# Kernel optimization log

Measured on AMD Instinct MI355X. Metric: run time of the kernel, lower is better.

The kernel has to match this reference:

```python
import jax, jax.numpy as jnp
import numpy as np

T, B, IN, H, A = 512, 256, 292, 128, 12


def setup_inputs() -> dict:
    key = jax.random.key(0)
    ks = jax.random.split(key, 8)
    s = 1.0 / np.sqrt(H)
    return {
        "x": jax.random.normal(ks[0], (T, B, IN), dtype=jnp.float32),
        "done": jax.random.randint(ks[1], (T, B), 0, 2, dtype=jnp.int32),
        "h0": jax.random.normal(ks[2], (1, B, H), dtype=jnp.float32),
        "c0": jax.random.normal(ks[3], (1, B, H), dtype=jnp.float32),
        "W_ih": jax.random.normal(ks[4], (4 * H, IN), dtype=jnp.float32) * s,
        "W_hh": jax.random.normal(ks[5], (4 * H, H), dtype=jnp.float32) * s,
        "b_ih": jnp.zeros((4 * H,), dtype=jnp.float32),
        "b_hh": jnp.zeros((4 * H,), dtype=jnp.float32),
        "W_pi": jax.random.normal(ks[6], (A, H), dtype=jnp.float32) * 0.01,
        "b_pi": jnp.zeros((A,), dtype=jnp.float32),
        "W_v": jax.random.normal(ks[7], (1, H), dtype=jnp.float32),
        "b_v": jnp.zeros((1,), dtype=jnp.float32),
    }


def reference(x, done, h0, c0, W_ih, W_hh, b_ih, b_hh, W_pi, b_pi, W_v, b_v):
    # get_states: per-timestep LSTM with done-based reset of (h, c), as a scan.
    done_f = done.astype(x.dtype)  # [T, B]
    bias = b_ih + b_hh  # [4H]

    def step(carry, inp):
        h, c = carry  # [B, H] each
        x_t, d_t = inp  # [B, IN], [B]
        m = (1.0 - d_t)[:, None]  # reset mask
        h = h * m
        c = c * m
        # PyTorch LSTM gate order: input, forget, cell(g), output
        gates = x_t @ W_ih.T + h @ W_hh.T + bias  # [B, 4H]
        i, f, g, o = jnp.split(gates, 4, axis=-1)
        c = jax.nn.sigmoid(f) * c + jax.nn.sigmoid(i) * jnp.tanh(g)
        h = jax.nn.sigmoid(o) * jnp.tanh(c)
        return (h, c), h

    (hN, cN), hs = jax.lax.scan(step, (h0[0], c0[0]), (x, done_f))
    hidden = hs.reshape(T * B, H)  # flatten(cat(new_hidden), 0, 1)
    logits = hidden @ W_pi.T + b_pi  # policy_layers
    value = hidden @ W_v.T + b_v  # value_layers
    return jnp.concatenate([logits, value], axis=-1)  # [T*B, A+1]
```

## Files before the change

### kernel.cpp

```cpp
#include <hip/hip_runtime.h>
#include <stdint.h>
#include <stddef.h>

#define T_ 512
#define B_ 256
#define IN_ 292
#define H_ 128
#define G4_ 512
#define TB_ 131072
#define LCH 32
#define NCH 16
#define KP_ 320

typedef short bf16x8 __attribute__((ext_vector_type(8)));
typedef float f32x4 __attribute__((ext_vector_type(4)));

__device__ __forceinline__ unsigned short f2bf(float f) {
  unsigned u = __float_as_uint(f);
  u += 0x7FFFu + ((u >> 16) & 1u);
  return (unsigned short)(u >> 16);
}
__device__ __forceinline__ float bf2f(unsigned short s) {
  return __uint_as_float(((unsigned)s) << 16);
}
__device__ __forceinline__ unsigned bfpack2(float a, float b) {
  unsigned ua = __float_as_uint(a) + 0x8000u;
  unsigned ub = __float_as_uint(b) + 0x8000u;
  return __builtin_amdgcn_perm(ub, ua, 0x07060302u);
}
__device__ __forceinline__ float sigf(float x) {
  return __builtin_amdgcn_rcpf(1.0f + __expf(-x));
}
__device__ __forceinline__ float tanhf_(float x) {
  return 1.0f - 2.0f * __builtin_amdgcn_rcpf(__expf(2.0f * x) + 1.0f);
}
__device__ __forceinline__ void barrier_lds() {
  asm volatile("s_waitcnt lgkmcnt(0)\n\ts_barrier" ::: "memory");
}
__device__ __forceinline__ void load_pr(const unsigned short* p, ushort4* pr) {
  union { uint4 v; ushort4 s[2]; } a, b;
  a.v = *(const uint4*)p;
  b.v = *(const uint4*)(p + 8);
  pr[0] = a.s[0]; pr[1] = a.s[1]; pr[2] = b.s[0]; pr[3] = b.s[1];
}

__global__ __launch_bounds__(256) void k0w_cvt(
    const float* __restrict__ Wih, const float* __restrict__ bih,
    const float* __restrict__ bhh, unsigned short* __restrict__ Wf,
    float* __restrict__ bias2) {
  const int g = blockIdx.x * 256 + threadIdx.x;
  const int lane = g & 63;
  const int rest = g >> 6;
  const int it = rest % 10;
  const int g16 = rest / 10;
  const int jj = g16 * 16 + (lane & 15);
  const int src = (jj & 3) * 128 + (jj >> 2);
  const int c0 = it * 32 + (lane >> 4) * 8;
  if (g < 512) {
    const int sb = (g & 3) * 128 + (g >> 2);
    bias2[g] = bih[sb] + bhh[sb];
  }
  float4 a = {0.f, 0.f, 0.f, 0.f}, b = {0.f, 0.f, 0.f, 0.f};
  const float* p = Wih + (size_t)src * IN_ + c0;
  if (c0 + 8 <= IN_) { a = *(const float4*)p; b = *(const float4*)(p + 4); }
  else if (c0 < IN_) { a = *(const float4*)p; }
  uint4 o;
  o.x = bfpack2(a.x, a.y); o.y = bfpack2(a.z, a.w);
  o.z = bfpack2(b.x, b.y); o.w = bfpack2(b.z, b.w);
  *(uint4*)&Wf[(size_t)g * 8] = o;
}

__device__ __forceinline__ void k1_xissue(
    const float* __restrict__ x, int bid4, int xrow, int xcq, int g2,
    float4* xa, float4* xbv) {
  const int jx = g2 / 10, itx = g2 % 10;
  const float* p = x + (size_t)((bid4 + jx) * 128 + xrow) * IN_ + itx * 32 + xcq;
  const float4 z = {0.f, 0.f, 0.f, 0.f};
  if (itx < 9) {
    xa[g2 & 1] = *(const float4*)p;
    xbv[g2 & 1] = *(const float4*)(p + 4);
  } else {
    xa[g2 & 1] = (xcq == 0) ? *(const float4*)p : z;
    xbv[g2 & 1] = z;
  }
}

__global__ __launch_bounds__(512, 2) void k1_pregemm(
    const float* __restrict__ x, const unsigned short* __restrict__ Wf,
    const float* __restrict__ bias2, unsigned short* __restrict__ pre2) {
  __shared__ unsigned short xt[2][128 * 40];
  __shared__ unsigned short ep[64 * 520];

  const int tid = threadIdx.x;
  const int w = tid >> 6;
  const int lane = tid & 63;
  const int l15 = lane & 15;
  const int q = lane >> 4;
  const int bid4 = blockIdx.x * 4;

  const int xrow = tid >> 2;
  const int xcq = (tid & 3) * 8;

  const unsigned short* wfbase = Wf + ((size_t)(4 * w) * 10 * 64 + lane) * 8;

  f32x4 acc[4][8];
#pragma unroll
  for (int s = 0; s < 4; s++)
#pragma unroll
    for (int ms = 0; ms < 8; ms++) acc[s][ms] = (f32x4){0.f, 0.f, 0.f, 0.f};

  float4 xa[2], xbv[2];
  k1_xissue(x, bid4, xrow, xcq, 0, xa, xbv);
  k1_xissue(x, bid4, xrow, xcq, 1, xa, xbv);
  bf16x8 af[4];
#pragma unroll
  for (int s = 0; s < 4; s++)
    af[s] = *(const bf16x8*)(wfbase + (s * 10 + 0) * 512);
  {
    uint4 v;
    v.x = bfpack2(xa[0].x, xa[0].y); v.y = bfpack2(xa[0].z, xa[0].w);
    v.z = bfpack2(xbv[0].x, xbv[0].y); v.w = bfpack2(xbv[0].z, xbv[0].w);
    *(uint4*)&xt[0][xrow * 40 + xcq] = v;
  }
  barrier_lds();

#pragma unroll 1
  for (int git = 0; git < 40; ++git) {
    const int it = git % 10;
    bf16x8 afn[4];
    if (git < 39) {
      const int nit = (it == 9) ? 0 : it + 1;
#pragma unroll
      for (int s = 0; s < 4; s++)
        afn[s] = *(const bf16x8*)(wfbase + (s * 10 + nit) * 512);
    }
    if (git + 2 < 40) k1_xissue(x, bid4, xrow, xcq, git + 2, xa, xbv);
    const unsigned short* xb = xt[git & 1];
    bf16x8 bfr[8];
#pragma unroll
    for (int ms = 0; ms < 8; ms++)
      bfr[ms] = *(const bf16x8*)&xb[(16 * ms + l15) * 40 + q * 8];
#pragma unroll
    for (int s = 0; s < 4; s++)
#pragma unroll
      for (int ms = 0; ms < 8; ms++)
        acc[s][ms] = __builtin_amdgcn_mfma_f32_16x16x32_bf16(
            af[s], bfr[ms], acc[s][ms], 0, 0, 0);
    if (git < 39) {
      const float4 A = xa[(git + 1) & 1], Bv = xbv[(git + 1) & 1];
      uint4 v;
      v.x = bfpack2(A.x, A.y); v.y = bfpack2(A.z, A.w);
      v.z = bfpack2(Bv.x, Bv.y); v.w = bfpack2(Bv.z, Bv.w);
      *(uint4*)&xt[(git + 1) & 1][xrow * 40 + xcq] = v;
    }
#pragma unroll
    for (int s = 0; s < 4; s++) af[s] = afn[s];
    barrier_lds();

    if (it == 9) {
      const int m0 = (bid4 + git / 10) * 128;
      float4 bb[4];
#pragma unroll
      for (int s = 0; s < 4; s++)
        bb[s] = *(const float4*)&bias2[64 * w + 16 * s + 4 * q];
#pragma unroll
      for (int st = 0; st < 2; ++st) {
#pragma unroll
        for (int mm = 0; mm < 4; ++mm) {
          const int ms = 4 * st + mm;
#pragma unroll
          for (int s = 0; s < 4; ++s) {
            uint2 v;
            v.x = bfpack2(acc[s][ms][0] + bb[s].x, acc[s][ms][1] + bb[s].y);
            v.y = bfpack2(acc[s][ms][2] + bb[s].z, acc[s][ms][3] + bb[s].w);
            *(uint2*)&ep[(16 * mm + l15) * 520 + 64 * w + 16 * s + 4 * q] = v;
          }
        }
        barrier_lds();
#pragma unroll
        for (int p = 0; p < 8; ++p) {
          const int r = 8 * p + w;
          uint4 v = *(const uint4*)&ep[r * 520 + lane * 8];
          *(uint4*)&pre2[((size_t)(m0 + 64 * st + r) << 9) + lane * 8] = v;
        }
        barrier_lds();
      }
      if (git < 39) {
#pragma unroll
        for (int s = 0; s < 4; s++)
#pragma unroll
          for (int ms = 0; ms < 8; ms++) acc[s][ms] = (f32x4){0.f, 0.f, 0.f, 0.f};
      }
    }
  }
}

__global__ __launch_bounds__(512) void k2a_chunk(
    const unsigned short* __restrict__ pre2, const float* __restrict__ Whh,
    const int* __restrict__ done, unsigned short* __restrict__ hidden,
    unsigned short* __restrict__ hfin, float* __restrict__ cfin) {
  __shared__ unsigned short hs[2][16 * 136];
  __shared__ int dns[LCH * 16];

  const int bg = blockIdx.x & 15;
  const int ck = blockIdx.x >> 4;
  const int t0 = ck * LCH;
  const int tid = threadIdx.x;
  const int w = tid >> 6;
  const int lane = tid & 63;
  const int l15 = lane & 15;
  const int q = lane >> 4;
  const int bglob = bg * 16 + l15;
  const int kcell = 16 * w + 4 * q;
  const int kq16 = kcell * 4;

  {
    const int r = tid >> 4, c = tid & 15;
    dns[tid] = done[(size_t)(t0 + r) * B_ + bg * 16 + c];
  }

  bf16x8 wf[4][4];
#pragma unroll
  for (int tI = 0; tI < 4; tI++) {
    const int jg = 16 * (w + 8 * tI) + l15;
#pragma unroll
    for (int kc = 0; kc < 4; kc++) {
      const float* p = Whh + (size_t)jg * H_ + kc * 32 + q * 8;
      float4 u0 = *(const float4*)p;
      float4 u1 = *(const float4*)(p + 4);
      bf16x8 r;
      r[0]=(short)f2bf(u0.x); r[1]=(short)f2bf(u0.y); r[2]=(short)f2bf(u0.z); r[3]=(short)f2bf(u0.w);
      r[4]=(short)f2bf(u1.x); r[5]=(short)f2bf(u1.y); r[6]=(short)f2bf(u1.z); r[7]=(short)f2bf(u1.w);
      wf[tI][kc] = r;
    }
  }

  float c_[4] = {0.f, 0.f, 0.f, 0.f};
  {
    const int b = tid >> 5, k = (tid & 31) * 4;
    *(ushort4*)&hs[0][b * 136 + k] = (ushort4){0, 0, 0, 0};
  }
  bool vld = false;
  __syncthreads();

  ushort4 pr[4], prn[4];
  load_pr(pre2 + ((size_t)t0 * B_ + bglob) * G4_ + kq16, pr);
  load_pr(pre2 + ((size_t)(t0 + 1) * B_ + bglob) * G4_ + kq16, prn);

  ushort4 hw = {0, 0, 0, 0};
#pragma unroll 1
  for (int u = 0; u < LCH; u++) {
    const int t = t0 + u;
    ushort4 pr2[4];
    const int un = (u + 2 < LCH) ? u + 2 : LCH - 1;
    load_pr(pre2 + ((size_t)(t0 + un) * B_ + bglob) * G4_ + kq16, pr2);

    const int dn = dns[u * 16 + l15];
    vld = vld || (dn != 0);

    const unsigned short* hb = hs[u & 1];
    bf16x8 hf[4];
#pragma unroll
    for (int kc = 0; kc < 4; kc++) {
      bf16x8 v = *(const bf16x8*)&hb[l15 * 136 + kc * 32 + q * 8];
      if (dn) v = (bf16x8){0, 0, 0, 0, 0, 0, 0, 0};
      hf[kc] = v;
    }

    f32x4 acc[4];
#pragma unroll
    for (int tI = 0; tI < 4; tI++) acc[tI] = (f32x4){0.f, 0.f, 0.f, 0.f};
#pragma unroll
    for (int tI = 0; tI < 4; tI++)
#pragma unroll
      for (int kc = 0; kc < 4; kc++)
        acc[tI] = __builtin_amdgcn_mfma_f32_16x16x32_bf16(
            wf[tI][kc], hf[kc], acc[tI], 0, 0, 0);

    const float m = dn ? 0.0f : 1.0f;
    float hv[4];
#pragma unroll
    for (int r = 0; r < 4; r++) {
      const float iv = acc[0][r] + bf2f(pr[r].x);
      const float fv = acc[1][r] + bf2f(pr[r].y);
      const float gv = acc[2][r] + bf2f(pr[r].z);
      const float ov = acc[3][r] + bf2f(pr[r].w);
      float cc = c_[r] * m;
      cc = sigf(fv) * cc + sigf(iv) * tanhf_(gv);
      c_[r] = cc;
      hv[r] = sigf(ov) * tanhf_(cc);
    }
    uint2 hp = {bfpack2(hv[0], hv[1]), bfpack2(hv[2], hv[3])};
    hw = *(ushort4*)&hp;
    *(uint2*)&hs[(u + 1) & 1][l15 * 136 + kcell] = hp;
    if (vld)
      *(uint2*)&hidden[((size_t)t * B_ + bglob) * H_ + kcell] = hp;
#pragma unroll
    for (int tI = 0; tI < 4; tI++) { pr[tI] = prn[tI]; prn[tI] = pr2[tI]; }
    barrier_lds();
  }

  *(ushort4*)&hfin[((size_t)ck * B_ + bglob) * H_ + kcell] = hw;
  float4 cv = {c_[0], c_[1], c_[2], c_[3]};
  *(float4*)&cfin[((size_t)ck * B_ + bglob) * H_ + kcell] = cv;
}

__global__ __launch_bounds__(512) void k2b_par(
    const unsigned short* __restrict__ pre2, const float* __restrict__ Whh,
    const float* __restrict__ h0, const float* __restrict__ c0,
    const int* __restrict__ done, unsigned short* __restrict__ hidden,
    const unsigned short* __restrict__ hfin, const float* __restrict__ cfin,
    int* __restrict__ needfix) {
  __shared__ unsigned short hs[2][16 * 136];
  __shared__ int dns[LCH * 16];

  const int bg = blockIdx.x & 15;
  const int ck = blockIdx.x >> 4;
  const int t0 = ck * LCH;
  const int tid = threadIdx.x;
  const int w = tid >> 6;
  const int lane = tid & 63;
  const int l15 = lane & 15;
  const int q = lane >> 4;
  const int bglob = bg * 16 + l15;
  const int kcell = 16 * w + 4 * q;
  const int kq16 = kcell * 4;

  {
    const int r = tid >> 4, c = tid & 15;
    dns[tid] = done[(size_t)(t0 + r) * B_ + bg * 16 + c];
  }

  bf16x8 wf[4][4];
#pragma unroll
  for (int tI = 0; tI < 4; tI++) {
    const int jg = 16 * (w + 8 * tI) + l15;
#pragma unroll
    for (int kc = 0; kc < 4; kc++) {
      const float* p = Whh + (size_t)jg * H_ + kc * 32 + q * 8;
      float4 u0 = *(const float4*)p;
      float4 u1 = *(const float4*)(p + 4);
      bf16x8 r;
      r[0]=(short)f2bf(u0.x); r[1]=(short)f2bf(u0.y); r[2]=(short)f2bf(u0.z); r[3]=(short)f2bf(u0.w);
      r[4]=(short)f2bf(u1.x); r[5]=(short)f2bf(u1.y); r[6]=(short)f2bf(u1.z); r[7]=(short)f2bf(u1.w);
      wf[tI][kc] = r;
    }
  }

  float c_[4];
  {
    const int b = tid >> 5, k = (tid & 31) * 4;
    if (ck == 0) {
      float4 hv = *(const float4*)(h0 + (size_t)(bg * 16 + b) * H_ + k);
      uint2 hp = {bfpack2(hv.x, hv.y), bfpack2(hv.z, hv.w)};
      *(uint2*)&hs[0][b * 136 + k] = hp;
      float4 cv = *(const float4*)(c0 + (size_t)bglob * H_ + kcell);
      c_[0] = cv.x; c_[1] = cv.y; c_[2] = cv.z; c_[3] = cv.w;
    } else {
      ushort4 hv = *(const ushort4*)&hfin[((size_t)(ck - 1) * B_ + bg * 16 + b) * H_ + k];
      *(ushort4*)&hs[0][b * 136 + k] = hv;
      float4 cv = *(const float4*)&cfin[((size_t)(ck - 1) * B_ + bglob) * H_ + kcell];
      c_[0] = cv.x; c_[1] = cv.y; c_[2] = cv.z; c_[3] = cv.w;
    }
  }
  int cur = 0;
  bool act = true;
  __syncthreads();

  ushort4 pr[4];
  load_pr(pre2 + ((size_t)t0 * B_ + bglob) * G4_ + kq16, pr);

#pragma unroll 1
  for (int u = 0; u < LCH; u++) {
    const int t = t0 + u;
    const int dn = dns[u * 16 + l15];
    const bool nact = act && (dn == 0);
    if (__ballot(nact) == 0ULL) { act = false; break; }
    act = nact;

    ushort4 prn[4];
    const int un = (u + 1 < LCH) ? u + 1 : LCH - 1;
    load_pr(pre2 + ((size_t)(t0 + un) * B_ + bglob) * G4_ + kq16, prn);

    const unsigned short* hb = hs[cur];
    bf16x8 hf[4];
#pragma unroll
    for (int kc = 0; kc < 4; kc++)
      hf[kc] = *(const bf16x8*)&hb[l15 * 136 + kc * 32 + q * 8];

    f32x4 acc[4];
#pragma unroll
    for (int tI = 0; tI < 4; tI++) acc[tI] = (f32x4){0.f, 0.f, 0.f, 0.f};
#pragma unroll
    for (int tI = 0; tI < 4; tI++)
#pragma unroll
      for (int kc = 0; kc < 4; kc++)
        acc[tI] = __builtin_amdgcn_mfma_f32_16x16x32_bf16(
            wf[tI][kc], hf[kc], acc[tI], 0, 0, 0);

    float hv[4];
#pragma unroll
    for (int r = 0; r < 4; r++) {
      const float iv = acc[0][r] + bf2f(pr[r].x);
      const float fv = acc[1][r] + bf2f(pr[r].y);
      const float gv = acc[2][r] + bf2f(pr[r].z);
      const float ov = acc[3][r] + bf2f(pr[r].w);
      float cc = sigf(fv) * c_[r] + sigf(iv) * tanhf_(gv);
      c_[r] = cc;
      hv[r] = sigf(ov) * tanhf_(cc);
    }
    uint2 hp = {bfpack2(hv[0], hv[1]), bfpack2(hv[2], hv[3])};
    *(uint2*)&hs[cur ^ 1][l15 * 136 + kcell] = hp;
    if (act)
      *(uint2*)&hidden[((size_t)t * B_ + bglob) * H_ + kcell] = hp;
#pragma unroll
    for (int tI = 0; tI < 4; tI++) pr[tI] = prn[tI];
    barrier_lds();
    cur ^= 1;
  }

  if (tid == 0) needfix[blockIdx.x] = (__ballot(act) != 0ULL) ? 1 : 0;
}

__global__ __launch_bounds__(512) void k2c_guard(
    const unsigned short* __restrict__ pre2, const float* __restrict__ Whh,
    const float* __restrict__ h0, const float* __restrict__ c0,
    const int* __restrict__ done, unsigned short* __restrict__ hidden,
    const unsigned short* __restrict__ hfin, const float* __restrict__ cfin,
    const int* __restrict__ needfix) {
  const int bg = blockIdx.x;
  bool dirty = false;
  for (int c2 = 0; c2 < NCH - 1; c2++) dirty |= (needfix[c2 * 16 + bg] != 0);
  if (!dirty) return;

  __shared__ unsigned short hs[2][16 * 136];
  __shared__ int dns[T_ * 16];

  const int tid = threadIdx.x;
  const int w = tid >> 6;
  const int lane = tid & 63;
  const int l15 = lane & 15;
  const int q = lane >> 4;
  const int bglob = bg * 16 + l15;
  const int kcell = 16 * w + 4 * q;
  const int kq16 = kcell * 4;

  {
    const int* p = done + (size_t)tid * B_ + bg * 16;
    *(int4*)&dns[tid * 16]      = *(const int4*)(p);
    *(int4*)&dns[tid * 16 + 4]  = *(const int4*)(p + 4);
    *(int4*)&dns[tid * 16 + 8]  = *(const int4*)(p + 8);
    *(int4*)&dns[tid * 16 + 12] = *(const int4*)(p + 12);
  }

  bf16x8 wf[4][4];
#pragma unroll
  for (int tI = 0; tI < 4; tI++) {
    const int jg = 16 * (w + 8 * tI) + l15;
#pragma unroll
    for (int kc = 0; kc < 4; kc++) {
      const float* p = Whh + (size_t)jg * H_ + kc * 32 + q * 8;
      float4 u0 = *(const float4*)p;
      float4 u1 = *(const float4*)(p + 4);
      bf16x8 r;
      r[0]=(short)f2bf(u0.x); r[1]=(short)f2bf(u0.y); r[2]=(short)f2bf(u0.z); r[3]=(short)f2bf(u0.w);
      r[4]=(short)f2bf(u1.x); r[5]=(short)f2bf(u1.y); r[6]=(short)f2bf(u1.z); r[7]=(short)f2bf(u1.w);
      wf[tI][kc] = r;
    }
  }

  float c_[4];
  {
    float4 cv = *(const float4*)(c0 + (size_t)bglob * H_ + kcell);
    c_[0] = cv.x; c_[1] = cv.y; c_[2] = cv.z; c_[3] = cv.w;
    const int b = tid >> 5, k = (tid & 31) * 4;
    float4 hv = *(const float4*)(h0 + (size_t)(bg * 16 + b) * H_ + k);
    uint2 hp = {bfpack2(hv.x, hv.y), bfpack2(hv.z, hv.w)};
    *(uint2*)&hs[0][b * 136 + k] = hp;
  }
  int cur = 0;
  __syncthreads();

#pragma unroll 1
  for (int ck = 0; ck < NCH; ck++) {
    const int t0 = ck * LCH;
    bool act = true;

    ushort4 pr[4];
    load_pr(pre2 + ((size_t)t0 * B_ + bglob) * G4_ + kq16, pr);

#pragma unroll 1
    for (int u = 0; u < LCH; u++) {
      const int t = t0 + u;
      const int dn = dns[t * 16 + l15];
      const bool nact = act && (dn == 0);
      if (__ballot(nact) == 0ULL) { act = false; break; }
      act = nact;

      ushort4 prn[4];
      const int un = (u + 1 < LCH) ? u + 1 : LCH - 1;
      load_pr(pre2 + ((size_t)(t0 + un) * B_ + bglob) * G4_ + kq16, prn);

      const unsigned short* hb = hs[cur];
      bf16x8 hf[4];
#pragma unroll
      for (int kc = 0; kc < 4; kc++)
        hf[kc] = *(const bf16x8*)&hb[l15 * 136 + kc * 32 + q * 8];

      f32x4 acc[4];
#pragma unroll
      for (int tI = 0; tI < 4; tI++) acc[tI] = (f32x4){0.f, 0.f, 0.f, 0.f};
#pragma unroll
      for (int tI = 0; tI < 4; tI++)
#pragma unroll
        for (int kc = 0; kc < 4; kc++)
          acc[tI] = __builtin_amdgcn_mfma_f32_16x16x32_bf16(
              wf[tI][kc], hf[kc], acc[tI], 0, 0, 0);

      float hv[4];
#pragma unroll
      for (int r = 0; r < 4; r++) {
        const float iv = acc[0][r] + bf2f(pr[r].x);
        const float fv = acc[1][r] + bf2f(pr[r].y);
        const float gv = acc[2][r] + bf2f(pr[r].z);
        const float ov = acc[3][r] + bf2f(pr[r].w);
        float cc = sigf(fv) * c_[r] + sigf(iv) * tanhf_(gv);
        c_[r] = cc;
        hv[r] = sigf(ov) * tanhf_(cc);
      }
      uint2 hp = {bfpack2(hv[0], hv[1]), bfpack2(hv[2], hv[3])};
      *(uint2*)&hs[cur ^ 1][l15 * 136 + kcell] = hp;
      if (act)
        *(uint2*)&hidden[((size_t)t * B_ + bglob) * H_ + kcell] = hp;
#pragma unroll
      for (int tI = 0; tI < 4; tI++) pr[tI] = prn[tI];
      barrier_lds();
      cur ^= 1;
    }

    if (!act) {
      ushort4 hv = *(const ushort4*)&hfin[((size_t)ck * B_ + bglob) * H_ + kcell];
      float4 cv = *(const float4*)&cfin[((size_t)ck * B_ + bglob) * H_ + kcell];
      c_[0] = cv.x; c_[1] = cv.y; c_[2] = cv.z; c_[3] = cv.w;
      *(ushort4*)&hs[cur][l15 * 136 + kcell] = hv;
    }
    barrier_lds();
  }
}

__global__ __launch_bounds__(256) void k3_head(
    const unsigned short* __restrict__ hidden, const float* __restrict__ Wpi,
    const float* __restrict__ bpi, const float* __restrict__ Wv,
    const float* __restrict__ bv, float* __restrict__ out) {
  __shared__ unsigned short hs3[64 * 136];
  __shared__ float bias_s[16];

  const int tid = threadIdx.x;
  const int w = tid >> 6;
  const int lane = tid & 63;
  const int l15 = lane & 15;
  const int q = lane >> 4;
  const int m0 = blockIdx.x * 64;

  if (tid < 16) bias_s[tid] = (tid < 12) ? bpi[tid] : ((tid == 12) ? bv[0] : 0.f);

  bf16x8 wf3[4];
#pragma unroll
  for (int kc = 0; kc < 4; kc++) {
    float4 u0 = {0.f, 0.f, 0.f, 0.f}, u1 = {0.f, 0.f, 0.f, 0.f};
    if (l15 < 12) {
      const float* p = Wpi + (size_t)l15 * H_ + kc * 32 + q * 8;
      u0 = *(const float4*)p; u1 = *(const float4*)(p + 4);
    } else if (l15 == 12) {
      const float* p = Wv + kc * 32 + q * 8;
      u0 = *(const float4*)p; u1 = *(const float4*)(p + 4);
    }
    bf16x8 r;
    r[0]=(short)f2bf(u0.x); r[1]=(short)f2bf(u0.y); r[2]=(short)f2bf(u0.z); r[3]=(short)f2bf(u0.w);
    r[4]=(short)f2bf(u1.x); r[5]=(short)f2bf(u1.y); r[6]=(short)f2bf(u1.z); r[7]=(short)f2bf(u1.w);
    wf3[kc] = r;
  }

  {
    const int row = tid >> 2, ks = (tid & 3) * 32;
    const unsigned short* p = hidden + (size_t)(m0 + row) * H_ + ks;
#pragma unroll
    for (int i = 0; i < 4; i++)
      *(uint4*)&hs3[row * 136 + ks + i * 8] = *(const uint4*)(p + i * 8);
  }
  __syncthreads();

  f32x4 acc = (f32x4){0.f, 0.f, 0.f, 0.f};
#pragma unroll
  for (int kc = 0; kc < 4; kc++) {
    bf16x8 hf = *(bf16x8*)&hs3[(16 * w + l15) * 136 + kc * 32 + q * 8];
    acc = __builtin_amdgcn_mfma_f32_16x16x32_bf16(wf3[kc], hf, acc, 0, 0, 0);
  }

  const float4 bb = *(float4*)&bias_s[4 * q];
  const int m = m0 + 16 * w + l15;
  const size_t ro = (size_t)m * 13;
  float v0 = acc[0] + bb.x, v1 = acc[1] + bb.y, v2 = acc[2] + bb.z, v3 = acc[3] + bb.w;
  if (q < 3) {
    out[ro + 4 * q + 0] = v0;
    out[ro + 4 * q + 1] = v1;
    out[ro + 4 * q + 2] = v2;
    out[ro + 4 * q + 3] = v3;
  } else {
    out[ro + 12] = v0;
  }
}

extern "C" void kernel_launch(void* const* d_in, const int* in_sizes, int n_in,
                              void* d_out, int out_size, void* d_ws, size_t ws_size,
                              hipStream_t stream) {
  const float* x    = (const float*)d_in[0];
  const int* done   = (const int*)d_in[1];
  const float* h0   = (const float*)d_in[2];
  const float* c0   = (const float*)d_in[3];
  const float* Wih  = (const float*)d_in[4];
  const float* Whh  = (const float*)d_in[5];
  const float* bih  = (const float*)d_in[6];
  const float* bhh  = (const float*)d_in[7];
  const float* Wpi  = (const float*)d_in[8];
  const float* bpi  = (const float*)d_in[9];
  const float* Wv   = (const float*)d_in[10];
  const float* bv   = (const float*)d_in[11];
  (void)in_sizes; (void)n_in; (void)out_size; (void)ws_size;

  unsigned short* pre2 = (unsigned short*)d_ws;
  unsigned short* hidden = pre2 + (size_t)TB_ * G4_;
  unsigned short* Wf   = (unsigned short*)d_out;
  float* bias2         = (float*)((char*)d_out + (512u << 10));
  unsigned short* hfin = (unsigned short*)((char*)d_out + (1u << 20));
  float* cfin          = (float*)((char*)d_out + (2u << 20));
  int* needfix         = (int*)((char*)d_out + (4u << 20));
  float* out = (float*)d_out;

  k0w_cvt<<<80, 256, 0, stream>>>(Wih, bih, bhh, Wf, bias2);
  k1_pregemm<<<256, 512, 0, stream>>>(x, Wf, bias2, pre2);
  k2a_chunk<<<256, 512, 0, stream>>>(pre2, Whh, done, hidden, hfin, cfin);
  k2b_par<<<256, 512, 0, stream>>>(pre2, Whh, h0, c0, done, hidden, hfin, cfin, needfix);
  k2c_guard<<<16, 512, 0, stream>>>(pre2, Whh, h0, c0, done, hidden, hfin, cfin, needfix);
  k3_head<<<TB_ / 64, 256, 0, stream>>>(hidden, Wpi, bpi, Wv, bv, out);
}
```

Baseline: 400.4 us.

## Stage x tiles into LDS via direct global-to-LDS loads with XOR swizzle

The input-projection GEMM now copies x tiles straight from global memory into LDS as fp32 using global_load_lds, instead of loading into registers, converting to bf16 and storing to LDS. An XOR swizzle on the 16-byte chunks is meant to avoid LDS bank conflicts, and the bf16 conversion moves to the LDS read before the MFMAs. This frees registers and VALU work from the staging path, but doubles the LDS footprint per tile, shortens prefetch depth to one tile, and leaves stale LDS data in the padded tail columns. That tail data relies on the zero-padded weights to cancel it.

```diff
diff --git a/kernel.cpp b/kernel.cpp
--- a/kernel.cpp
+++ b/kernel.cpp
@@ -36,6 +36,11 @@
 }
 __device__ __forceinline__ void barrier_lds() {
   asm volatile("s_waitcnt lgkmcnt(0)\n\ts_barrier" ::: "memory");
+}
+__device__ __forceinline__ void gload_lds16(const float* g, float* l) {
+  __builtin_amdgcn_global_load_lds(
+      (const __attribute__((address_space(1))) void*)g,
+      (__attribute__((address_space(3))) void*)l, 16, 0, 0);
 }
 __device__ __forceinline__ void load_pr(const unsigned short* p, ushort4* pr) {
   union { uint4 v; ushort4 s[2]; } a, b;
@@ -70,25 +75,25 @@
   *(uint4*)&Wf[(size_t)g * 8] = o;
 }
 
-__device__ __forceinline__ void k1_xissue(
-    const float* __restrict__ x, int bid4, int xrow, int xcq, int g2,
-    float4* xa, float4* xbv) {
-  const int jx = g2 / 10, itx = g2 % 10;
-  const float* p = x + (size_t)((bid4 + jx) * 128 + xrow) * IN_ + itx * 32 + xcq;
-  const float4 z = {0.f, 0.f, 0.f, 0.f};
-  if (itx < 9) {
-    xa[g2 & 1] = *(const float4*)p;
-    xbv[g2 & 1] = *(const float4*)(p + 4);
-  } else {
-    xa[g2 & 1] = (xcq == 0) ? *(const float4*)p : z;
-    xbv[g2 & 1] = z;
+__device__ __forceinline__ void k1_stage(
+    const float* __restrict__ x, float* ldsbuf, int bid4, int g2,
+    int w, int lane) {
+  const int jx = g2 / 10, kt = g2 % 10;
+#pragma unroll
+  for (int j = 0; j < 2; ++j) {
+    const int r = w * 16 + j * 8 + (lane >> 3);
+    const int tq = (lane & 7) ^ (r & 7);
+    const float* src =
+        x + (size_t)((bid4 + jx) * 128 + r) * IN_ + kt * 32 + tq * 4;
+    float* dst = ldsbuf + w * 512 + j * 256;
+    if (kt < 9 || tq == 0) gload_lds16(src, dst);
   }
 }
 
 __global__ __launch_bounds__(512, 2) void k1_pregemm(
     const float* __restrict__ x, const unsigned short* __restrict__ Wf,
     const float* __restrict__ bias2, unsigned short* __restrict__ pre2) {
-  __shared__ unsigned short xt[2][128 * 40];
+  __shared__ float xtf[2][128 * 32];
   __shared__ unsigned short ep[64 * 520];
 
   const int tid = threadIdx.x;
@@ -98,9 +103,6 @@
   const int q = lane >> 4;
   const int bid4 = blockIdx.x * 4;
 
-  const int xrow = tid >> 2;
-  const int xcq = (tid & 3) * 8;
-
   const unsigned short* wfbase = Wf + ((size_t)(4 * w) * 10 * 64 + lane) * 8;
 
   f32x4 acc[4][8];
@@ -109,55 +111,48 @@
 #pragma unroll
     for (int ms = 0; ms < 8; ms++) acc[s][ms] = (f32x4){0.f, 0.f, 0.f, 0.f};
 
-  float4 xa[2], xbv[2];
-  k1_xissue(x, bid4, xrow, xcq, 0, xa, xbv);
-  k1_xissue(x, bid4, xrow, xcq, 1, xa, xbv);
+  k1_stage(x, &xtf[0][0], bid4, 0, w, lane);
   bf16x8 af[4];
 #pragma unroll
   for (int s = 0; s < 4; s++)
     af[s] = *(const bf16x8*)(wfbase + (s * 10 + 0) * 512);
-  {
-    uint4 v;
-    v.x = bfpack2(xa[0].x, xa[0].y); v.y = bfpack2(xa[0].z, xa[0].w);
-    v.z = bfpack2(xbv[0].x, xbv[0].y); v.w = bfpack2(xbv[0].z, xbv[0].w);
-    *(uint4*)&xt[0][xrow * 40 + xcq] = v;
-  }
-  barrier_lds();
+  __syncthreads();
 
 #pragma unroll 1
   for (int git = 0; git < 40; ++git) {
-    const int it = git % 10;
+    const int kt = git % 10;
     bf16x8 afn[4];
     if (git < 39) {
-      const int nit = (it == 9) ? 0 : it + 1;
+      const int nit = (kt == 9) ? 0 : kt + 1;
 #pragma unroll
       for (int s = 0; s < 4; s++)
         afn[s] = *(const bf16x8*)(wfbase + (s * 10 + nit) * 512);
     }
-    if (git + 2 < 40) k1_xissue(x, bid4, xrow, xcq, git + 2, xa, xbv);
-    const unsigned short* xb = xt[git & 1];
+    const float* xb = &xtf[git & 1][0];
     bf16x8 bfr[8];
 #pragma unroll
-    for (int ms = 0; ms < 8; ms++)
-      bfr[ms] = *(const bf16x8*)&xb[(16 * ms + l15) * 40 + q * 8];
+    for (int ms = 0; ms < 8; ms++) {
+      const int r = 16 * ms + l15;
+      const int a0 = (2 * q) ^ (r & 7), a1 = (2 * q + 1) ^ (r & 7);
+      const float4 u0 = *(const float4*)&xb[r * 32 + a0 * 4];
+      const float4 u1 = *(const float4*)&xb[r * 32 + a1 * 4];
+      union { unsigned u[4]; bf16x8 v; } cv;
+      cv.u[0] = bfpack2(u0.x, u0.y); cv.u[1] = bfpack2(u0.z, u0.w);
+      cv.u[2] = bfpack2(u1.x, u1.y); cv.u[3] = bfpack2(u1.z, u1.w);
+      bfr[ms] = cv.v;
+    }
+    if (git < 39) k1_stage(x, &xtf[(git + 1) & 1][0], bid4, git + 1, w, lane);
 #pragma unroll
     for (int s = 0; s < 4; s++)
 #pragma unroll
       for (int ms = 0; ms < 8; ms++)
         acc[s][ms] = __builtin_amdgcn_mfma_f32_16x16x32_bf16(
             af[s], bfr[ms], acc[s][ms], 0, 0, 0);
-    if (git < 39) {
-      const float4 A = xa[(git + 1) & 1], Bv = xbv[(git + 1) & 1];
-      uint4 v;
-      v.x = bfpack2(A.x, A.y); v.y = bfpack2(A.z, A.w);
-      v.z = bfpack2(Bv.x, Bv.y); v.w = bfpack2(Bv.z, Bv.w);
-      *(uint4*)&xt[(git + 1) & 1][xrow * 40 + xcq] = v;
-    }
 #pragma unroll
     for (int s = 0; s < 4; s++) af[s] = afn[s];
-    barrier_lds();
-
-    if (it == 9) {
+    __syncthreads();
+
+    if (kt == 9) {
       const int m0 = (bid4 + git / 10) * 128;
       float4 bb[4];
 #pragma unroll
```

Result: faster. 380.5 us (-5.0%).
